# Kernel optimization log

Measured on AMD Instinct MI355X. Metric: run time of the kernel, lower is better.

Reference implementation:

```python
import jax, jax.numpy as jnp
import numpy as np

H_DIM = 1024
N_HEADS = 16
MAX_T = 2048
NUM_INPUTS = 3   # period of (return, state, action) tokens
RET_ORDER = 2


def _build_mask(T):
    # causal lower-triangular mask with mgdt selective column masking
    mask = jnp.tril(jnp.ones((T, T), dtype=bool))
    # columns period+ret_order-1, period+ret_order-1+period, ... are zeroed
    cols = np.arange(NUM_INPUTS + RET_ORDER - 1, MAX_T, NUM_INPUTS)
    cols = cols[cols < T]
    mask = mask.at[:, cols].set(False)
    return mask  # [T, T] bool


def setup_inputs() -> dict:
    key = jax.random.key(0)
    ks = jax.random.split(key, 9)
    B, T, C = 2, 2048, H_DIM
    s = 1.0 / np.sqrt(C)
    return {
        "x": jax.random.normal(ks[0], (B, T, C), dtype=jnp.float32),
        "Wq": jax.random.normal(ks[1], (C, C), dtype=jnp.float32) * s,
        "bq": jnp.zeros((C,), dtype=jnp.float32),
        "Wk": jax.random.normal(ks[2], (C, C), dtype=jnp.float32) * s,
        "bk": jnp.zeros((C,), dtype=jnp.float32),
        "Wv": jax.random.normal(ks[3], (C, C), dtype=jnp.float32) * s,
        "bv": jnp.zeros((C,), dtype=jnp.float32),
        "Wp": jax.random.normal(ks[4], (C, C), dtype=jnp.float32) * s,
        "bp": jnp.zeros((C,), dtype=jnp.float32),
    }


def reference(x, Wq, bq, Wk, bk, Wv, bv, Wp, bp):
    B, T, C = x.shape
    N = N_HEADS
    D = C // N
    # QKV projections; weights stored (in, out) so x @ W
    q = (x @ Wq + bq).reshape(B, T, N, D).transpose(0, 2, 1, 3)  # [B,N,T,D]
    k = (x @ Wk + bk).reshape(B, T, N, D).transpose(0, 2, 1, 3)
    v = (x @ Wv + bv).reshape(B, T, N, D).transpose(0, 2, 1, 3)

    scale = 1.0 / np.sqrt(D).astype(np.float32)
    scores = jnp.einsum("bntd,bnsd->bnts", q, k) * scale  # [B,N,T,T]
    mask = _build_mask(T)  # [T,T]
    scores = jnp.where(mask[None, None], scores, -jnp.inf)
    attn = jax.nn.softmax(scores, axis=-1)
    out = jnp.einsum("bnts,bnsd->bntd", attn, v)  # [B,N,T,D]
    out = out.transpose(0, 2, 1, 3).reshape(B, T, C)
    return out @ Wp + bp
```

## Files before the change

### kernel.cpp

```cpp
#include <hip/hip_runtime.h>

#define AS_GLOBAL __attribute__((address_space(1)))
#define AS_LDS    __attribute__((address_space(3)))

typedef __bf16 bf16;
typedef __bf16 bf16x4 __attribute__((ext_vector_type(4)));
typedef __bf16 bf16x8 __attribute__((ext_vector_type(8)));
typedef float  f32x4  __attribute__((ext_vector_type(4)));
typedef unsigned short u16x8 __attribute__((ext_vector_type(8)));

__device__ __forceinline__ void gload16(const void* g, void* l) {
  __builtin_amdgcn_global_load_lds((const AS_GLOBAL unsigned int*)g,
                                   (AS_LDS unsigned int*)l, 16, 0, 0);
}

__device__ __forceinline__ void* swz(void* base, int row, int bytecol) {
  return (char*)base + row * 128 + (bytecol ^ ((row & 7) << 4));
}

__device__ __forceinline__ int keptcnt(int X) { return X - ((X - 2) < 0 ? 0 : (X - 2) / 3); }
__device__ __forceinline__ int ci2s(int ci) {
  return 3 * ((ci - 2) >> 1) + 2 + ((ci - 2) & 1);
}
__device__ __forceinline__ int ci2s_full(int ci) {
  return ci < 2 ? ci : ci2s(ci);
}


__global__ __launch_bounds__(256) void k_cvt_bf16(const float* __restrict__ x,
                                                  bf16* __restrict__ o, int n8) {
  int i = blockIdx.x * blockDim.x + threadIdx.x;
  if (i >= n8) return;
  const float4* p = (const float4*)(x + (size_t)i * 8);
  float4 a = p[0], b = p[1];
  bf16x8 v;
  v[0] = (bf16)a.x; v[1] = (bf16)a.y; v[2] = (bf16)a.z; v[3] = (bf16)a.w;
  v[4] = (bf16)b.x; v[5] = (bf16)b.y; v[6] = (bf16)b.z; v[7] = (bf16)b.w;
  *(bf16x8*)(o + (size_t)i * 8) = v;
}

__global__ __launch_bounds__(256) void k_wt(const float* __restrict__ W,
                                            bf16* __restrict__ WT) {
  int lin = blockIdx.x * blockDim.x + threadIdx.x;
  int n  = lin & 1023;
  int kc = lin >> 10;
  bf16x8 v;
#pragma unroll
  for (int j = 0; j < 8; ++j) v[j] = (bf16)W[(size_t)(kc * 8 + j) * 1024 + n];
  *(bf16x8*)&WT[(size_t)n * 1024 + kc * 8] = v;
}

__global__ __launch_bounds__(256) void k_bcat(const float* __restrict__ bq,
                                              const float* __restrict__ bk,
                                              const float* __restrict__ bv,
                                              float* __restrict__ bc) {
  int i = blockIdx.x * blockDim.x + threadIdx.x;
  if (i < 1024) bc[i] = bq[i];
  else if (i < 2048) bc[i] = bk[i - 1024];
  else if (i < 3072) bc[i] = bv[i - 2048];
}

__global__ __launch_bounds__(256) void k_compact_k(const bf16* __restrict__ qkv,
                                                   bf16* __restrict__ kc) {
  int blk = blockIdx.x;
  int bh = blk / 44, rc = blk % 44;
  int b = bh >> 4, h = bh & 15;
  int rr = threadIdx.x >> 3, ch = threadIdx.x & 7;
  int ci = rc * 32 + rr;
  int s = ci2s_full(ci);
  bf16x8 v = {};
  if (s < 2048)
    v = *(const bf16x8*)&qkv[(size_t)(b * 2048 + s) * 3072 + 1024 + h * 64 + ch * 8];
  *(bf16x8*)&kc[((size_t)bh * 1408 + ci) * 64 + ch * 8] = v;
}

__global__ __launch_bounds__(256) void k_compact_v(const bf16* __restrict__ qkv,
                                                   bf16* __restrict__ vc) {
  __shared__ unsigned L[32 * 65];
  int blk = blockIdx.x;
  int bh = blk / 22, cc = blk % 22;
  int b = bh >> 4, h = bh & 15;
  int ci0 = cc * 64;
  int tid = threadIdx.x;
  int p = tid >> 3, d0 = (tid & 7) * 8;
  int s0 = ci2s_full(ci0 + 2 * p), s1 = ci2s_full(ci0 + 2 * p + 1);
  u16x8 e = {}, od = {};
  if (s0 < 2048)
    e = *(const u16x8*)&qkv[(size_t)(b * 2048 + s0) * 3072 + 2048 + h * 64 + d0];
  if (s1 < 2048)
    od = *(const u16x8*)&qkv[(size_t)(b * 2048 + s1) * 3072 + 2048 + h * 64 + d0];
#pragma unroll
  for (int k2 = 0; k2 < 8; ++k2)
    L[p * 65 + d0 + k2] = (unsigned)e[k2] | ((unsigned)od[k2] << 16);
  __syncthreads();
#pragma unroll
  for (int it = 0; it < 2; ++it) {
    int d = it * 32 + (tid >> 3), jg = tid & 7;
    unsigned q4[4];
#pragma unroll
    for (int jj = 0; jj < 4; ++jj) q4[jj] = L[(jg * 4 + jj) * 65 + d];
    *(uint4*)&vc[((size_t)bh * 64 + d) * 1408 + ci0 + jg * 8] = *(uint4*)q4;
  }
}

template <typename OutT>
__global__ __launch_bounds__(256) void k_gemm_bt(const bf16* __restrict__ A,
                                                 const bf16* __restrict__ Bt,
                                                 const float* __restrict__ bias,
                                                 OutT* __restrict__ C,
                                                 int K, int N) {
  __shared__ bf16 As[2][128 * 32];
  __shared__ bf16 Bs[2][128 * 32];
  const int tid = threadIdx.x;
  const int w = tid >> 6, l = tid & 63, g = l >> 4, c = l & 15;
  const int wr = w >> 1, wc = w & 1;
  int lin = blockIdx.y * gridDim.x + blockIdx.x;
  int chunk = (gridDim.x * gridDim.y) >> 3;
  int nl = (lin & 7) * chunk + (lin >> 3);
  const int row0 = (nl % gridDim.x) * 128, col0 = (nl / gridDim.x) * 128;
  f32x4 acc[4][4] = {};

  auto stage = [&](int buf, int k0) {
#pragma unroll
    for (int it = 0; it < 2; ++it) {
      int idx = it * 256 + tid;
      int r = idx >> 2, cc = idx & 3;
      int jj = cc ^ ((r >> 1) & 3);
      gload16(A  + (size_t)(row0 + r) * K + k0 + jj * 8, &As[buf][idx * 8]);
      gload16(Bt + (size_t)(col0 + r) * K + k0 + jj * 8, &Bs[buf][idx * 8]);
    }
  };

  stage(0, 0);
  int cur = 0;
#pragma unroll 1
  for (int k0 = 0; k0 < K; k0 += 32) {
    asm volatile("s_waitcnt vmcnt(0)" ::: "memory");
    __builtin_amdgcn_sched_barrier(0);
    __builtin_amdgcn_s_barrier();
    __builtin_amdgcn_sched_barrier(0);

    if (k0 + 32 < K) stage(cur ^ 1, k0 + 32);

    bf16x8 af[4], bfr[4];
#pragma unroll
    for (int m = 0; m < 4; ++m) {
      int row = wr * 64 + m * 16 + c;
      af[m] = *(const bf16x8*)&As[cur][row * 32 + (g ^ ((row >> 1) & 3)) * 8];
    }
#pragma unroll
    for (int n = 0; n < 4; ++n) {
      int row = wc * 64 + n * 16 + c;
      bfr[n] = *(const bf16x8*)&Bs[cur][row * 32 + (g ^ ((row >> 1) & 3)) * 8];
    }
#pragma unroll
    for (int m = 0; m < 4; ++m)
#pragma unroll
      for (int n = 0; n < 4; ++n)
        acc[m][n] = __builtin_amdgcn_mfma_f32_16x16x32_bf16(af[m], bfr[n],
                                                            acc[m][n], 0, 0, 0);
    cur ^= 1;
  }

#pragma unroll
  for (int m = 0; m < 4; ++m) {
    int row = row0 + wr * 64 + m * 16 + g * 4;
#pragma unroll
    for (int n = 0; n < 4; ++n) {
      int col = col0 + wc * 64 + n * 16 + c;
      float bv = bias[col];
#pragma unroll
      for (int r = 0; r < 4; ++r) {
        float v = acc[m][n][r] + bv;
        C[(size_t)(row + r) * N + col] = (OutT)v;
      }
    }
  }
}

__global__ __launch_bounds__(256, 4) void k_attn(const bf16* __restrict__ qkv,
                                                 const bf16* __restrict__ kc,
                                                 const bf16* __restrict__ vc,
                                                 bf16* __restrict__ att) {
  const int idx = blockIdx.x;
  const int slot = idx >> 8, j = idx & 255;
  const int r8 = j >> 5, bh = j & 31;
  const int b = bh >> 4, h = bh & 15;
  int qt;
  switch (slot) {
    case 0: qt = r8;       break;
    case 1: qt = 31 - r8;  break;
    case 2: qt = r8 + 8;   break;
    default: qt = 23 - r8; break;
  }

  const int tid = threadIdx.x;
  const int w = tid >> 6, l = tid & 63, g = l >> 4, c = l & 15;
  const int qw0 = qt * 64 + w * 16;
  const int qq = qw0 + c;

  const int nt = (keptcnt(qt * 64 + 64) + 63) >> 6;
  const int tmaskw = keptcnt(qw0 + 1) >> 6;

  __shared__ bf16 Ks[2][64 * 64];
  __shared__ bf16 Vs[2][64 * 64];
  __shared__ bf16 Plds[4][16 * 64];

  const bf16* kgc = kc + (size_t)bh * 1408 * 64;
  const bf16* vgc = vc + (size_t)bh * 64 * 1408;

  auto stage = [&](int buf, int t) {
    int s0 = t * 64;
#pragma unroll
    for (int it = 0; it < 2; ++it) {
      int ch = it * 256 + tid;
      int rr = ch >> 3, jj = (ch & 7) ^ (rr & 7);
      gload16(kgc + (size_t)(s0 + rr) * 64 + jj * 8, &Ks[buf][ch * 8]);
      gload16(vgc + (size_t)rr * 1408 + s0 + jj * 8, &Vs[buf][ch * 8]);
    }
  };

  const bf16* qb = qkv + (size_t)(b * 2048 + qq) * 3072 + h * 64 + g * 8;
  bf16x8 qf0 = *(const bf16x8*)qb;
  bf16x8 qf1 = *(const bf16x8*)(qb + 32);
#pragma unroll
  for (int jq = 0; jq < 8; ++jq) {
    qf0[jq] = (bf16)((float)qf0[jq] * 0.125f);
    qf1[jq] = (bf16)((float)qf1[jq] * 0.125f);
  }

  f32x4 o[4] = {};
  float mrow = -1e30f, ell = 0.f;

  stage(0, 0);

  int cur = 0;
#pragma unroll 1
  for (int t = 0; t < nt; ++t) {
    asm volatile("s_waitcnt vmcnt(0)" ::: "memory");
    __builtin_amdgcn_sched_barrier(0);
    __builtin_amdgcn_s_barrier();
    __builtin_amdgcn_sched_barrier(0);

    if (t + 1 < nt) stage(cur ^ 1, t + 1);

    f32x4 ss[4] = {};
#pragma unroll
    for (int st = 0; st < 4; ++st) {
      bf16x8 ka  = *(const bf16x8*)swz(&Ks[cur][0], st * 16 + c, g * 16);
      bf16x8 kb2 = *(const bf16x8*)swz(&Ks[cur][0], st * 16 + c, 64 + g * 16);
      ss[st] = __builtin_amdgcn_mfma_f32_16x16x32_bf16(ka,  qf0, ss[st], 0, 0, 0);
      ss[st] = __builtin_amdgcn_mfma_f32_16x16x32_bf16(kb2, qf1, ss[st], 0, 0, 0);
    }

    float mloc = -1e30f;
    if (t >= tmaskw) {
#pragma unroll
      for (int st = 0; st < 4; ++st)
#pragma unroll
        for (int r = 0; r < 4; ++r) {
          int ci = t * 64 + st * 16 + g * 4 + r;
          int s = ci2s(ci);
          if (t == 0) s = (ci < 2) ? ci : s;
          float v = (s <= qq) ? ss[st][r] : -1e30f;
          ss[st][r] = v;
          mloc = fmaxf(mloc, v);
        }
    } else {
#pragma unroll
      for (int st = 0; st < 4; ++st)
#pragma unroll
        for (int r = 0; r < 4; ++r) mloc = fmaxf(mloc, ss[st][r]);
    }
    mloc = fmaxf(mloc, __shfl_xor(mloc, 16));
    mloc = fmaxf(mloc, __shfl_xor(mloc, 32));

    float mn = fmaxf(mrow, mloc);
    float al = __expf(mrow - mn);
    mrow = mn;
    float rsum = 0.f;
#pragma unroll
    for (int st = 0; st < 4; ++st) {
      float p0 = __expf(ss[st][0] - mn);
      float p1 = __expf(ss[st][1] - mn);
      float p2 = __expf(ss[st][2] - mn);
      float p3 = __expf(ss[st][3] - mn);
      rsum += (p0 + p1) + (p2 + p3);
      bf16x4 pk = {(bf16)p0, (bf16)p1, (bf16)p2, (bf16)p3};
      *(bf16x4*)swz(&Plds[w][0], c, st * 32 + g * 8) = pk;
    }
    rsum += __shfl_xor(rsum, 16);
    rsum += __shfl_xor(rsum, 32);
    ell = ell * al + rsum;
#pragma unroll
    for (int dc = 0; dc < 4; ++dc)
#pragma unroll
      for (int r = 0; r < 4; ++r) o[dc][r] *= al;

    asm volatile("s_waitcnt lgkmcnt(0)" ::: "memory");
    __builtin_amdgcn_sched_barrier(0);

#pragma unroll
    for (int kk = 0; kk < 2; ++kk) {
      bf16x8 pf = *(const bf16x8*)swz(&Plds[w][0], c, kk * 64 + g * 16);
#pragma unroll
      for (int dc = 0; dc < 4; ++dc) {
        bf16x8 vf = *(const bf16x8*)swz(&Vs[cur][0], dc * 16 + c, kk * 64 + g * 16);
        o[dc] = __builtin_amdgcn_mfma_f32_16x16x32_bf16(vf, pf, o[dc], 0, 0, 0);
      }
    }

    cur ^= 1;
  }

  float inv = 1.f / ell;
#pragma unroll
  for (int dc = 0; dc < 4; ++dc) {
    bf16x4 ok4 = {(bf16)(o[dc][0] * inv), (bf16)(o[dc][1] * inv),
                  (bf16)(o[dc][2] * inv), (bf16)(o[dc][3] * inv)};
    *(bf16x4*)swz(&Plds[w][0], c, dc * 32 + g * 8) = ok4;
  }
  asm volatile("s_waitcnt lgkmcnt(0)" ::: "memory");
  __builtin_amdgcn_sched_barrier(0);
#pragma unroll
  for (int p = 0; p < 2; ++p) {
    int row = p * 8 + (l >> 3);
    bf16x8 vrow = *(const bf16x8*)swz(&Plds[w][0], row, (l & 7) * 16);
    *(bf16x8*)&att[(size_t)(b * 2048 + qt * 64 + w * 16 + row) * 1024 +
                   h * 64 + (l & 7) * 8] = vrow;
  }
}

extern "C" void kernel_launch(void* const* d_in, const int* in_sizes, int n_in,
                              void* d_out, int out_size, void* d_ws, size_t ws_size,
                              hipStream_t stream) {
  const float* x  = (const float*)d_in[0];
  const float* Wq = (const float*)d_in[1];
  const float* bq = (const float*)d_in[2];
  const float* Wk = (const float*)d_in[3];
  const float* bk = (const float*)d_in[4];
  const float* Wv = (const float*)d_in[5];
  const float* bv = (const float*)d_in[6];
  const float* Wp = (const float*)d_in[7];
  const float* bp = (const float*)d_in[8];
  float* out = (float*)d_out;

  char* ws = (char*)d_ws;
  const size_t MB = 1024 * 1024;
  bf16*  xb    = (bf16*)(ws);
  bf16*  wqkvT = (bf16*)(ws + 8 * MB);
  bf16*  wpT   = (bf16*)(ws + 14 * MB);
  float* bcat  = (float*)(ws + 16 * MB);
  bf16*  qkv   = (bf16*)(ws + 17 * MB);
  bf16*  kcb   = wqkvT;
  bf16*  vcb   = (bf16*)(ws + 41 * MB);
  bf16*  att   = xb;

  k_cvt_bf16<<<2048, 256, 0, stream>>>(x, xb, 524288);
  k_wt<<<512, 256, 0, stream>>>(Wq, wqkvT);
  k_wt<<<512, 256, 0, stream>>>(Wk, wqkvT + 1024 * 1024);
  k_wt<<<512, 256, 0, stream>>>(Wv, wqkvT + 2 * 1024 * 1024);
  k_wt<<<512, 256, 0, stream>>>(Wp, wpT);
  k_bcat<<<12, 256, 0, stream>>>(bq, bk, bv, bcat);

  k_gemm_bt<bf16><<<dim3(32, 24), 256, 0, stream>>>(xb, wqkvT, bcat, qkv, 1024, 3072);
  k_compact_k<<<1408, 256, 0, stream>>>(qkv, kcb);
  k_compact_v<<<704, 256, 0, stream>>>(qkv, vcb);
  k_attn<<<1024, 256, 0, stream>>>(qkv, kcb, vcb, att);
  k_gemm_bt<float><<<dim3(32, 8), 256, 0, stream>>>(att, wpT, bp, out, 1024, 1024);
}
```

Before: 119.1 us.

## Use 256x256-tile 8-wave GEMM with staged double-buffered loads for QKV projection

Replaces the QKV projection GEMM with a new kernel that uses 256x256 output tiles, 512 threads (8 waves) and double-buffered LDS. The next k-tile's global-to-LDS loads are split into four phases interleaved with MFMA groups, with explicit waitcnt, setprio and barriers. It also adds an XCD-aware block remapping. The larger tile is meant to raise data reuse and overlap memory with compute, but the grid shrinks to 192 blocks, which can leave some of the CUs underused, and the kernel uses 128KB of LDS.

```diff
diff --git a/kernel.cpp b/kernel.cpp
--- a/kernel.cpp
+++ b/kernel.cpp
@@ -178,6 +178,131 @@
   }
 }
 
+template <typename OutT>
+__global__ __launch_bounds__(512) void k_gemm8(const bf16* __restrict__ A,
+                                               const bf16* __restrict__ Bt,
+                                               const float* __restrict__ bias,
+                                               OutT* __restrict__ C,
+                                               int K, int N, int mblocks) {
+  __shared__ bf16 As[2][256 * 64];
+  __shared__ bf16 Bs[2][256 * 64];
+  const int tid = threadIdx.x;
+  const int l = tid & 63, g = l >> 4, c = l & 15;
+  const int w = tid >> 6, wr = w >> 2, wc = w & 3;
+  int lin = blockIdx.x;
+  int nl = (lin & 7) * (gridDim.x >> 3) + (lin >> 3);
+  const int row0 = (nl % mblocks) * 256, col0 = (nl / mblocks) * 256;
+
+  const int rr = tid >> 3, jg = tid & 7;
+  const int jj = jg ^ (rr & 7);
+
+  auto stage_hs = [&](int buf, int kt, int p) {
+    if (p < 2) {
+      int r0 = p * 128 + rr, r1 = p * 128 + 64 + rr;
+      gload16(Bt + (size_t)(col0 + r0) * K + kt * 64 + jj * 8, &Bs[buf][r0 * 64 + jg * 8]);
+      gload16(Bt + (size_t)(col0 + r1) * K + kt * 64 + jj * 8, &Bs[buf][r1 * 64 + jg * 8]);
+    } else {
+      int r0 = (p - 2) * 64 + rr, r1 = 128 + (p - 2) * 64 + rr;
+      gload16(A + (size_t)(row0 + r0) * K + kt * 64 + jj * 8, &As[buf][r0 * 64 + jg * 8]);
+      gload16(A + (size_t)(row0 + r1) * K + kt * 64 + jj * 8, &As[buf][r1 * 64 + jg * 8]);
+    }
+  };
+
+  f32x4 acc[8][4] = {};
+  bf16x8 bfr[4][2];
+  const int NT = K >> 6;
+
+#pragma unroll
+  for (int p = 0; p < 4; ++p) stage_hs(0, 0, p);
+  asm volatile("s_waitcnt vmcnt(2)" ::: "memory");
+  __builtin_amdgcn_sched_barrier(0);
+  __builtin_amdgcn_s_barrier();
+
+#pragma unroll 1
+  for (int t = 0; t < NT; ++t) {
+    const int cur = t & 1;
+    const bool nxt = (t + 1 < NT);
+    bf16* Asc = &As[cur][0];
+    bf16* Bsc = &Bs[cur][0];
+
+    {
+#pragma unroll
+      for (int n = 0; n < 4; ++n) {
+        int row = wc * 64 + n * 16 + c;
+#pragma unroll
+        for (int kk = 0; kk < 2; ++kk)
+          bfr[n][kk] = *(const bf16x8*)&Bsc[row * 64 + ((kk * 4 + g) ^ (c & 7)) * 8];
+      }
+      bf16x8 af[2][2];
+#pragma unroll
+      for (int i = 0; i < 2; ++i) {
+        int row = wr * 128 + i * 16 + c;
+#pragma unroll
+        for (int kk = 0; kk < 2; ++kk)
+          af[i][kk] = *(const bf16x8*)&Asc[row * 64 + ((kk * 4 + g) ^ (c & 7)) * 8];
+      }
+      if (nxt) stage_hs(cur ^ 1, t + 1, 0);
+      asm volatile("s_waitcnt lgkmcnt(0)" ::: "memory");
+      __builtin_amdgcn_sched_barrier(0);
+      __builtin_amdgcn_s_setprio(1);
+#pragma unroll
+      for (int i = 0; i < 2; ++i)
+#pragma unroll
+        for (int n = 0; n < 4; ++n)
+#pragma unroll
+          for (int kk = 0; kk < 2; ++kk)
+            acc[i][n] = __builtin_amdgcn_mfma_f32_16x16x32_bf16(af[i][kk], bfr[n][kk], acc[i][n], 0, 0, 0);
+      __builtin_amdgcn_s_setprio(0);
+      __builtin_amdgcn_s_barrier();
+    }
+#pragma unroll
+    for (int p = 1; p < 4; ++p) {
+      bf16x8 af[2][2];
+#pragma unroll
+      for (int i = 0; i < 2; ++i) {
+        int row = wr * 128 + (2 * p + i) * 16 + c;
+#pragma unroll
+        for (int kk = 0; kk < 2; ++kk)
+          af[i][kk] = *(const bf16x8*)&Asc[row * 64 + ((kk * 4 + g) ^ (c & 7)) * 8];
+      }
+      if (nxt) stage_hs(cur ^ 1, t + 1, p);
+      asm volatile("s_waitcnt lgkmcnt(0)" ::: "memory");
+      __builtin_amdgcn_sched_barrier(0);
+      __builtin_amdgcn_s_setprio(1);
+#pragma unroll
+      for (int i = 0; i < 2; ++i)
+#pragma unroll
+        for (int n = 0; n < 4; ++n)
+#pragma unroll
+          for (int kk = 0; kk < 2; ++kk)
+            acc[2 * p + i][n] = __builtin_amdgcn_mfma_f32_16x16x32_bf16(af[i][kk], bfr[n][kk], acc[2 * p + i][n], 0, 0, 0);
+      __builtin_amdgcn_s_setprio(0);
+      if (p == 1) {
+        if (nxt) { asm volatile("s_waitcnt vmcnt(4)" ::: "memory"); }
+        else     { asm volatile("s_waitcnt vmcnt(0)" ::: "memory"); }
+        __builtin_amdgcn_sched_barrier(0);
+      } else if (p == 3) {
+        if (nxt) { asm volatile("s_waitcnt vmcnt(2)" ::: "memory"); }
+        __builtin_amdgcn_sched_barrier(0);
+      }
+      __builtin_amdgcn_s_barrier();
+    }
+  }
+
+#pragma unroll
+  for (int mi = 0; mi < 8; ++mi) {
+    int row = row0 + wr * 128 + mi * 16 + g * 4;
+#pragma unroll
+    for (int n = 0; n < 4; ++n) {
+      int col = col0 + wc * 64 + n * 16 + c;
+      float bv = bias[col];
+#pragma unroll
+      for (int r = 0; r < 4; ++r)
+        C[(size_t)(row + r) * N + col] = (OutT)(acc[mi][n][r] + bv);
+    }
+  }
+}
+
 __global__ __launch_bounds__(256, 4) void k_attn(const bf16* __restrict__ qkv,
                                                  const bf16* __restrict__ kc,
                                                  const bf16* __restrict__ vc,
@@ -363,7 +488,7 @@
   k_wt<<<512, 256, 0, stream>>>(Wp, wpT);
   k_bcat<<<12, 256, 0, stream>>>(bq, bk, bv, bcat);
 
-  k_gemm_bt<bf16><<<dim3(32, 24), 256, 0, stream>>>(xb, wqkvT, bcat, qkv, 1024, 3072);
+  k_gemm8<bf16><<<192, 512, 0, stream>>>(xb, wqkvT, bcat, qkv, 1024, 3072, 16);
   k_compact_k<<<1408, 256, 0, stream>>>(qkv, kcb);
   k_compact_v<<<704, 256, 0, stream>>>(qkv, vcb);
   k_attn<<<1024, 256, 0, stream>>>(qkv, kcb, vcb, att);
```

New measurement: 119.8 us. No clear change (+0.6%).

## Project K/V only for unmasked rows by gathering x before GEMM

Applied to the files above, without the earlier changes.

Instead of computing K and V for all 2048 tokens and then compacting, the kept rows of x are gathered first (1408 per batch) and a separate GEMM computes K|V only for those rows, writing directly in the compacted layout. Q gets its own GEMM. This removes about a third of the K/V projection FLOPs and the separate K compaction pass. The weight-transpose and bias-concat launches are merged into one kernel to cut launch overhead. In exchange it adds an x gather kernel, and attention now reads K with a 2048-element stride.

```diff
diff --git a/kernel.cpp b/kernel.cpp
--- a/kernel.cpp
+++ b/kernel.cpp
@@ -39,43 +39,46 @@
   *(bf16x8*)(o + (size_t)i * 8) = v;
 }
 
-__global__ __launch_bounds__(256) void k_wt(const float* __restrict__ W,
-                                            bf16* __restrict__ WT) {
-  int lin = blockIdx.x * blockDim.x + threadIdx.x;
-  int n  = lin & 1023;
-  int kc = lin >> 10;
+__global__ __launch_bounds__(256) void k_wt_all(const float* __restrict__ Wq,
+                                                const float* __restrict__ Wk,
+                                                const float* __restrict__ Wv,
+                                                const float* __restrict__ Wp,
+                                                const float* __restrict__ bq,
+                                                const float* __restrict__ bk,
+                                                const float* __restrict__ bv,
+                                                bf16* __restrict__ wqkvT,
+                                                bf16* __restrict__ wpT,
+                                                float* __restrict__ bc) {
+  int blk = blockIdx.x;
+  if (blk >= 2048) {
+    int i = (blk - 2048) * 256 + threadIdx.x;
+    bc[i] = (i < 1024) ? bq[i] : (i < 2048 ? bk[i - 1024] : bv[i - 2048]);
+    return;
+  }
+  int sel = blk >> 9;
+  const float* W = (sel == 0) ? Wq : (sel == 1) ? Wk : (sel == 2) ? Wv : Wp;
+  bf16* dst = (sel < 3) ? (wqkvT + (size_t)sel * 1024 * 1024) : wpT;
+  int lin = (blk & 511) * 256 + threadIdx.x;
+  int n = lin & 1023, kc = lin >> 10;
   bf16x8 v;
 #pragma unroll
   for (int j = 0; j < 8; ++j) v[j] = (bf16)W[(size_t)(kc * 8 + j) * 1024 + n];
-  *(bf16x8*)&WT[(size_t)n * 1024 + kc * 8] = v;
-}
-
-__global__ __launch_bounds__(256) void k_bcat(const float* __restrict__ bq,
-                                              const float* __restrict__ bk,
-                                              const float* __restrict__ bv,
-                                              float* __restrict__ bc) {
-  int i = blockIdx.x * blockDim.x + threadIdx.x;
-  if (i < 1024) bc[i] = bq[i];
-  else if (i < 2048) bc[i] = bk[i - 1024];
-  else if (i < 3072) bc[i] = bv[i - 2048];
-}
-
-__global__ __launch_bounds__(256) void k_compact_k(const bf16* __restrict__ qkv,
-                                                   bf16* __restrict__ kc) {
-  int blk = blockIdx.x;
-  int bh = blk / 44, rc = blk % 44;
-  int b = bh >> 4, h = bh & 15;
-  int rr = threadIdx.x >> 3, ch = threadIdx.x & 7;
-  int ci = rc * 32 + rr;
+  *(bf16x8*)&dst[(size_t)n * 1024 + kc * 8] = v;
+}
+
+__global__ __launch_bounds__(256) void k_xgather(const bf16* __restrict__ xb,
+                                                 bf16* __restrict__ xc) {
+  int idx = blockIdx.x * 256 + threadIdx.x;
+  int row = idx >> 7, gr = idx & 127;
+  int b = row / 1408, ci = row % 1408;
   int s = ci2s_full(ci);
   bf16x8 v = {};
-  if (s < 2048)
-    v = *(const bf16x8*)&qkv[(size_t)(b * 2048 + s) * 3072 + 1024 + h * 64 + ch * 8];
-  *(bf16x8*)&kc[((size_t)bh * 1408 + ci) * 64 + ch * 8] = v;
-}
-
-__global__ __launch_bounds__(256) void k_compact_v(const bf16* __restrict__ qkv,
-                                                   bf16* __restrict__ vc) {
+  if (s < 2048) v = *(const bf16x8*)&xb[(size_t)(b * 2048 + s) * 1024 + gr * 8];
+  *(bf16x8*)&xc[(size_t)row * 1024 + gr * 8] = v;
+}
+
+__global__ __launch_bounds__(256) void k_vtrans(const bf16* __restrict__ kvc,
+                                                bf16* __restrict__ vc) {
   __shared__ unsigned L[32 * 65];
   int blk = blockIdx.x;
   int bh = blk / 22, cc = blk % 22;
@@ -83,12 +86,9 @@
   int ci0 = cc * 64;
   int tid = threadIdx.x;
   int p = tid >> 3, d0 = (tid & 7) * 8;
-  int s0 = ci2s_full(ci0 + 2 * p), s1 = ci2s_full(ci0 + 2 * p + 1);
-  u16x8 e = {}, od = {};
-  if (s0 < 2048)
-    e = *(const u16x8*)&qkv[(size_t)(b * 2048 + s0) * 3072 + 2048 + h * 64 + d0];
-  if (s1 < 2048)
-    od = *(const u16x8*)&qkv[(size_t)(b * 2048 + s1) * 3072 + 2048 + h * 64 + d0];
+  const bf16* src = kvc + (size_t)(b * 1408 + ci0 + 2 * p) * 2048 + 1024 + h * 64 + d0;
+  u16x8 e  = *(const u16x8*)src;
+  u16x8 od = *(const u16x8*)(src + 2048);
 #pragma unroll
   for (int k2 = 0; k2 < 8; ++k2)
     L[p * 65 + d0 + k2] = (unsigned)e[k2] | ((unsigned)od[k2] << 16);
@@ -178,8 +178,8 @@
   }
 }
 
-__global__ __launch_bounds__(256, 4) void k_attn(const bf16* __restrict__ qkv,
-                                                 const bf16* __restrict__ kc,
+__global__ __launch_bounds__(256, 4) void k_attn(const bf16* __restrict__ qbuf,
+                                                 const bf16* __restrict__ kvc,
                                                  const bf16* __restrict__ vc,
                                                  bf16* __restrict__ att) {
   const int idx = blockIdx.x;
@@ -206,7 +206,7 @@
   __shared__ bf16 Vs[2][64 * 64];
   __shared__ bf16 Plds[4][16 * 64];
 
-  const bf16* kgc = kc + (size_t)bh * 1408 * 64;
+  const bf16* kgc = kvc + (size_t)b * 1408 * 2048 + h * 64;
   const bf16* vgc = vc + (size_t)bh * 64 * 1408;
 
   auto stage = [&](int buf, int t) {
@@ -215,12 +215,12 @@
     for (int it = 0; it < 2; ++it) {
       int ch = it * 256 + tid;
       int rr = ch >> 3, jj = (ch & 7) ^ (rr & 7);
-      gload16(kgc + (size_t)(s0 + rr) * 64 + jj * 8, &Ks[buf][ch * 8]);
+      gload16(kgc + (size_t)(s0 + rr) * 2048 + jj * 8, &Ks[buf][ch * 8]);
       gload16(vgc + (size_t)rr * 1408 + s0 + jj * 8, &Vs[buf][ch * 8]);
     }
   };
 
-  const bf16* qb = qkv + (size_t)(b * 2048 + qq) * 3072 + h * 64 + g * 8;
+  const bf16* qb = qbuf + (size_t)(b * 2048 + qq) * 1024 + h * 64 + g * 8;
   bf16x8 qf0 = *(const bf16x8*)qb;
   bf16x8 qf1 = *(const bf16x8*)(qb + 32);
 #pragma unroll
@@ -351,21 +351,20 @@
   bf16*  wqkvT = (bf16*)(ws + 8 * MB);
   bf16*  wpT   = (bf16*)(ws + 14 * MB);
   float* bcat  = (float*)(ws + 16 * MB);
-  bf16*  qkv   = (bf16*)(ws + 17 * MB);
-  bf16*  kcb   = wqkvT;
-  bf16*  vcb   = (bf16*)(ws + 41 * MB);
+  bf16*  qbuf  = (bf16*)(ws + 17 * MB);
+  bf16*  kvc   = (bf16*)(ws + 25 * MB);
+  bf16*  vcb   = (bf16*)(ws + 36 * MB);
+  bf16*  xcb   = (bf16*)(ws + 42 * MB);
   bf16*  att   = xb;
 
   k_cvt_bf16<<<2048, 256, 0, stream>>>(x, xb, 524288);
-  k_wt<<<512, 256, 0, stream>>>(Wq, wqkvT);
-  k_wt<<<512, 256, 0, stream>>>(Wk, wqkvT + 1024 * 1024);
-  k_wt<<<512, 256, 0, stream>>>(Wv, wqkvT + 2 * 1024 * 1024);
-  k_wt<<<512, 256, 0, stream>>>(Wp, wpT);
-  k_bcat<<<12, 256, 0, stream>>>(bq, bk, bv, bcat);
-
-  k_gemm_bt<bf16><<<dim3(32, 24), 256, 0, stream>>>(xb, wqkvT, bcat, qkv, 1024, 3072);
-  k_compact_k<<<1408, 256, 0, stream>>>(qkv, kcb);
-  k_compact_v<<<704, 256, 0, stream>>>(qkv, vcb);
-  k_attn<<<1024, 256, 0, stream>>>(qkv, kcb, vcb, att);
+  k_wt_all<<<2060, 256, 0, stream>>>(Wq, Wk, Wv, Wp, bq, bk, bv, wqkvT, wpT, bcat);
+  k_xgather<<<1408, 256, 0, stream>>>(xb, xcb);
+
+  k_gemm_bt<bf16><<<dim3(32, 8), 256, 0, stream>>>(xb, wqkvT, bcat, qbuf, 1024, 1024);
+  k_gemm_bt<bf16><<<dim3(22, 16), 256, 0, stream>>>(xcb, wqkvT + 1024 * 1024,
+                                                    bcat + 1024, kvc, 1024, 2048);
+  k_vtrans<<<704, 256, 0, stream>>>(kvc, vcb);
+  k_attn<<<1024, 256, 0, stream>>>(qbuf, kvc, vcb, att);
   k_gemm_bt<float><<<dim3(32, 8), 256, 0, stream>>>(att, wpT, bp, out, 1024, 1024);
 }
```

Result: slower. 127.3 us (+6.9%).
